# Kernel tuning notes

Measured on AMD Instinct MI355X. Metric: run time of the kernel, lower is better.

Reference implementation:

```python
import jax, jax.numpy as jnp
import numpy as np

N = 100000  # nodes
E = 320000  # edges
G = 64      # graphs in the batch


def setup_inputs() -> dict:
    key = jax.random.key(0)
    ks = jax.random.split(key, 16)
    inp = {
        "x": jax.random.normal(ks[0], (N, 512), dtype=jnp.float32),
        "edge_index": jax.random.randint(ks[1], (2, E), 0, N, dtype=jnp.int64),
        "batch": jnp.sort(jax.random.randint(ks[2], (N,), 0, G, dtype=jnp.int64)),
    }
    # GCNConv weights (in, out) and biases, Glorot-ish scale
    dims = [(512, 256), (256, 128), (128, 64), (64, 32)]
    for i, (din, dout) in enumerate(dims):
        inp[f"w{i+1}"] = jax.random.normal(ks[3 + i], (din, dout), dtype=jnp.float32) / np.sqrt(din)
        inp[f"b{i+1}"] = jnp.zeros((dout,), dtype=jnp.float32)
    inp["lw1"] = jax.random.normal(ks[8], (32, 16), dtype=jnp.float32) / np.sqrt(32.0)
    inp["lb1"] = jnp.zeros((16,), dtype=jnp.float32)
    inp["lw2"] = jax.random.normal(ks[9], (16, 2), dtype=jnp.float32) / np.sqrt(16.0)
    inp["lb2"] = jnpp = jnp.zeros((2,), dtype=jnp.float32)
    return inp


def _gcn_conv(h_in, w, b, src, dst, norm, n):
    # x' = D^-1/2 (A+I) D^-1/2 (X W) + b   (PyG GCNConv default)
    h = h_in @ w                                  # [N, out]
    msg = h[src] * norm[:, None]                  # gather + scale over edges(+self-loops)
    out = jax.ops.segment_sum(msg, dst, num_segments=n)  # scatter-add
    return out + b


def reference(x, edge_index, batch, w1, b1, w2, b2, w3, b3, w4, b4, lw1, lb1, lw2, lb2):
    n = x.shape[0]
    loop = jnp.arange(n, dtype=edge_index.dtype)
    src = jnp.concatenate([edge_index[0], loop])  # add self-loops
    dst = jnp.concatenate([edge_index[1], loop])
    # symmetric normalization: deg counted at dst (col) including self-loops
    deg = jax.ops.segment_sum(jnp.ones_like(dst, dtype=x.dtype), dst, num_segments=n)
    dinv = jnp.where(deg > 0, 1.0 / jnp.sqrt(deg), 0.0)
    norm = dinv[src] * dinv[dst]                  # [E+N]

    h = jax.nn.relu(_gcn_conv(x, w1, b1, src, dst, norm, n))
    h = jax.nn.relu(_gcn_conv(h, w2, b2, src, dst, norm, n))
    h = jax.nn.relu(_gcn_conv(h, w3, b3, src, dst, norm, n))
    h = _gcn_conv(h, w4, b4, src, dst, norm, n)   # [N, 32]

    # global mean pool over graphs
    sums = jax.ops.segment_sum(h, batch, num_segments=G)
    cnt = jax.ops.segment_sum(jnp.ones((n,), dtype=h.dtype), batch, num_segments=G)
    pooled = sums / jnp.maximum(cnt, 1.0)[:, None]  # [G, 32]

    # dropout p=0.8 is identity in eval mode
    out = jax.nn.relu(pooled @ lw1 + lb1) @ lw2 + lb2  # [G, 2]
    return out
```

## Files before the change

### kernel.cpp

```cpp
#include <hip/hip_runtime.h>
#include <cstdint>
#include <cstddef>


typedef __attribute__((ext_vector_type(8))) short s16x8;
typedef __attribute__((ext_vector_type(4))) float f32x4;

__device__ __forceinline__ short2 split2(float f) {
    union { float f; unsigned u; } c; c.f = f;
    short hi = (short)(c.u >> 16);
    union { unsigned u; float f; } h; h.u = c.u & 0xffff0000u;
    union { float f; unsigned u; } r; r.f = f - h.f;
    short lo = (short)(r.u >> 16);
    return make_short2(hi, lo);
}


__global__ void k_count(const int* __restrict__ dst, int E, int* __restrict__ cnt) {
    int e = blockIdx.x * blockDim.x + threadIdx.x;
    if (e < E) atomicAdd(&cnt[dst[e]], 1);
}

__global__ void k_dinv(const int* __restrict__ cnt, int n, float* __restrict__ dinv) {
    int i = blockIdx.x * blockDim.x + threadIdx.x;
    if (i < n) dinv[i] = rsqrtf((float)(cnt[i] + 1));
}


__global__ void k_scan_sums(const int* __restrict__ cnt, int n, int* __restrict__ bsum) {
    __shared__ int s[256];
    int t = threadIdx.x;
    int base = blockIdx.x * 4096 + t * 16;
    int sum = 0;
#pragma unroll
    for (int j = 0; j < 16; ++j) { int i = base + j; if (i < n) sum += cnt[i]; }
    s[t] = sum;
    __syncthreads();
    for (int off = 128; off > 0; off >>= 1) {
        if (t < off) s[t] += s[t + off];
        __syncthreads();
    }
    if (t == 0) bsum[blockIdx.x] = s[0];
}

__global__ void k_scan_offsets(const int* __restrict__ bsum, int nb,
                               int* __restrict__ boff, int* __restrict__ totalp) {
    int t = threadIdx.x;
    int v = (t < nb) ? bsum[t] : 0;
    int x = v;
    for (int off = 1; off < 64; off <<= 1) {
        int y = __shfl_up(x, off);
        if (t >= off) x += y;
    }
    if (t < nb) boff[t] = x - v;
    if (t == 63) *totalp = x;
}

__global__ void k_scan_final(const int* __restrict__ cnt, int n,
                             const int* __restrict__ boff, int* __restrict__ row_ptr) {
    __shared__ int s[256];
    int t = threadIdx.x;
    int base = blockIdx.x * 4096 + t * 16;
    int v[16]; int sum = 0;
#pragma unroll
    for (int j = 0; j < 16; ++j) { int i = base + j; v[j] = (i < n) ? cnt[i] : 0; sum += v[j]; }
    s[t] = sum;
    __syncthreads();
    for (int off = 1; off < 256; off <<= 1) {
        int y = (t >= off) ? s[t - off] : 0;
        __syncthreads();
        s[t] += y;
        __syncthreads();
    }
    int run = boff[blockIdx.x] + ((t == 0) ? 0 : s[t - 1]);
#pragma unroll
    for (int j = 0; j < 16; ++j) {
        int i = base + j;
        if (i < n) row_ptr[i] = run;
        run += v[j];
    }
}

__global__ void k_fill(const int* __restrict__ src, const int* __restrict__ dst, int E,
                       const int* __restrict__ row_ptr, int* __restrict__ cursor,
                       int* __restrict__ csr_src) {
    int e = blockIdx.x * blockDim.x + threadIdx.x;
    if (e >= E) return;
    int d = dst[e];
    int p = atomicAdd(&cursor[d], 1);
    csr_src[row_ptr[d] + p] = src[e];
}


#define SWZ(row, kbyte) ((((row) * 64)) ^ (kbyte) ^ (((row) & 7) << 4))

template <int FM, int FN, int GM, int GN>
__global__ __launch_bounds__(256)
void k_gemm_mfma(const float* __restrict__ A, const float* __restrict__ B,
                 float* __restrict__ C, int M, int K, int N) {
    constexpr int BM = GM * FM * 16;
    constexpr int BN = GN * FN * 16;
    constexpr int BK = 32;
    constexpr int ASZ = BM * BK * 2;
    constexpr int BSZ = BN * BK * 2;
    __shared__ char lds[2 * ASZ + 2 * BSZ];
    char* sAh = lds;
    char* sAl = lds + ASZ;
    char* sBh = lds + 2 * ASZ;
    char* sBl = lds + 2 * ASZ + BSZ;

    const int tid  = threadIdx.x;
    const int lane = tid & 63;
    const int wid  = tid >> 6;
    const int wm   = wid % GM;
    const int wn   = wid / GM;
    const int brow = blockIdx.y * BM;
    const int bcol = blockIdx.x * BN;
    const int l15  = lane & 15;
    const int kb   = ((lane >> 4) * 8) * 2;

    f32x4 acc[FM][FN];
#pragma unroll
    for (int i = 0; i < FM; ++i)
#pragma unroll
        for (int j = 0; j < FN; ++j) acc[i][j] = (f32x4){0.f, 0.f, 0.f, 0.f};

    for (int k0 = 0; k0 < K; k0 += BK) {
#pragma unroll
        for (int slot = tid; slot < BM * 2; slot += 256) {
            int row = slot >> 1, half = slot & 1;
            int gr = brow + row;
            float4 v0, v1, v2, v3;
            if (gr < M) {
                const float4* ap = (const float4*)(A + (size_t)gr * K + k0 + half * 16);
                v0 = ap[0]; v1 = ap[1]; v2 = ap[2]; v3 = ap[3];
            } else {
                v0 = v1 = v2 = v3 = make_float4(0.f, 0.f, 0.f, 0.f);
            }
            s16x8 h0, h1, l0, l1;
            short2 p;
            p = split2(v0.x); h0[0] = p.x; l0[0] = p.y;
            p = split2(v0.y); h0[1] = p.x; l0[1] = p.y;
            p = split2(v0.z); h0[2] = p.x; l0[2] = p.y;
            p = split2(v0.w); h0[3] = p.x; l0[3] = p.y;
            p = split2(v1.x); h0[4] = p.x; l0[4] = p.y;
            p = split2(v1.y); h0[5] = p.x; l0[5] = p.y;
            p = split2(v1.z); h0[6] = p.x; l0[6] = p.y;
            p = split2(v1.w); h0[7] = p.x; l0[7] = p.y;
            p = split2(v2.x); h1[0] = p.x; l1[0] = p.y;
            p = split2(v2.y); h1[1] = p.x; l1[1] = p.y;
            p = split2(v2.z); h1[2] = p.x; l1[2] = p.y;
            p = split2(v2.w); h1[3] = p.x; l1[3] = p.y;
            p = split2(v3.x); h1[4] = p.x; l1[4] = p.y;
            p = split2(v3.y); h1[5] = p.x; l1[5] = p.y;
            p = split2(v3.z); h1[6] = p.x; l1[6] = p.y;
            p = split2(v3.w); h1[7] = p.x; l1[7] = p.y;
            int base = half * 32;
            *(s16x8*)(sAh + SWZ(row, base))      = h0;
            *(s16x8*)(sAh + SWZ(row, base + 16)) = h1;
            *(s16x8*)(sAl + SWZ(row, base))      = l0;
            *(s16x8*)(sAl + SWZ(row, base + 16)) = l1;
        }
#pragma unroll
        for (int slot = tid; slot < BN * 2; slot += 256) {
            int col = slot >> 1, half = slot & 1;
            const float* bp = B + (size_t)(k0 + half * 16) * N + bcol + col;
            s16x8 h0, h1, l0, l1;
#pragma unroll
            for (int j = 0; j < 8; ++j) {
                short2 p = split2(bp[(size_t)j * N]);
                h0[j] = p.x; l0[j] = p.y;
            }
#pragma unroll
            for (int j = 0; j < 8; ++j) {
                short2 p = split2(bp[(size_t)(8 + j) * N]);
                h1[j] = p.x; l1[j] = p.y;
            }
            int base = half * 32;
            *(s16x8*)(sBh + SWZ(col, base))      = h0;
            *(s16x8*)(sBh + SWZ(col, base + 16)) = h1;
            *(s16x8*)(sBl + SWZ(col, base))      = l0;
            *(s16x8*)(sBl + SWZ(col, base + 16)) = l1;
        }
        __syncthreads();

        s16x8 ah[FM], am[FM], bh[FN], bm[FN];
#pragma unroll
        for (int i = 0; i < FM; ++i) {
            int row = wm * FM * 16 + i * 16 + l15;
            ah[i] = *(const s16x8*)(sAh + SWZ(row, kb));
            am[i] = *(const s16x8*)(sAl + SWZ(row, kb));
        }
#pragma unroll
        for (int j = 0; j < FN; ++j) {
            int col = wn * FN * 16 + j * 16 + l15;
            bh[j] = *(const s16x8*)(sBh + SWZ(col, kb));
            bm[j] = *(const s16x8*)(sBl + SWZ(col, kb));
        }
#pragma unroll
        for (int i = 0; i < FM; ++i)
#pragma unroll
            for (int j = 0; j < FN; ++j) {
                acc[i][j] = __builtin_amdgcn_mfma_f32_16x16x32_bf16(ah[i], bh[j], acc[i][j], 0, 0, 0);
                acc[i][j] = __builtin_amdgcn_mfma_f32_16x16x32_bf16(am[i], bh[j], acc[i][j], 0, 0, 0);
                acc[i][j] = __builtin_amdgcn_mfma_f32_16x16x32_bf16(ah[i], bm[j], acc[i][j], 0, 0, 0);
            }
        __syncthreads();
    }

#pragma unroll
    for (int i = 0; i < FM; ++i) {
#pragma unroll
        for (int r = 0; r < 4; ++r) {
            int row = brow + wm * FM * 16 + i * 16 + (lane >> 4) * 4 + r;
            if (row >= M) continue;
#pragma unroll
            for (int j = 0; j < FN; ++j) {
                int col = bcol + wn * FN * 16 + j * 16 + l15;
                C[(size_t)row * N + col] = acc[i][j][r];
            }
        }
    }
}


__global__ void k_agg(const float4* __restrict__ h, const int* __restrict__ row_ptr,
                      const int* __restrict__ csr_src, const float* __restrict__ dinv,
                      const float* __restrict__ bias, float4* __restrict__ out,
                      int n, int f_shift, int do_relu) {
    int idx = blockIdx.x * blockDim.x + threadIdx.x;
    int dout4 = 1 << f_shift;
    int total = n << f_shift;
    if (idx >= total) return;
    int i = idx >> f_shift;
    int f = idx & (dout4 - 1);

    float di = dinv[i];
    float4 hv = h[(size_t)i * dout4 + f];
    float4 acc;
    acc.x = hv.x * di; acc.y = hv.y * di; acc.z = hv.z * di; acc.w = hv.w * di;

    int s0 = row_ptr[i], s1 = row_ptr[i + 1];
    for (int e = s0; e < s1; ++e) {
        int s = csr_src[e];
        float ds = dinv[s];
        float4 v = h[(size_t)s * dout4 + f];
        acc.x += v.x * ds; acc.y += v.y * ds; acc.z += v.z * ds; acc.w += v.w * ds;
    }
    const float4* b4 = (const float4*)bias;
    float4 b = b4[f];
    float4 o;
    o.x = acc.x * di + b.x;
    o.y = acc.y * di + b.y;
    o.z = acc.z * di + b.z;
    o.w = acc.w * di + b.w;
    if (do_relu) {
        o.x = fmaxf(o.x, 0.f); o.y = fmaxf(o.y, 0.f);
        o.z = fmaxf(o.z, 0.f); o.w = fmaxf(o.w, 0.f);
    }
    out[(size_t)i * dout4 + f] = o;
}


__global__ void k_pool(const float* __restrict__ h, const int* __restrict__ batch,
                       int n, float* __restrict__ pooled) {
    int g = blockIdx.x;
    int start, end;
    {
        int lo = 0, hi = n;
        while (lo < hi) { int mid = (lo + hi) >> 1; if (batch[mid] < g) lo = mid + 1; else hi = mid; }
        start = lo;
        lo = start; hi = n;
        while (lo < hi) { int mid = (lo + hi) >> 1; if (batch[mid] < g + 1) lo = mid + 1; else hi = mid; }
        end = lo;
    }
    int f = threadIdx.x & 31;
    int sub = threadIdx.x >> 5;
    float s = 0.f;
    for (int i = start + sub; i < end; i += 8) s += h[(size_t)i * 32 + f];
    __shared__ float red[8][32];
    red[sub][f] = s;
    __syncthreads();
    if (sub == 0) {
        float t = 0.f;
#pragma unroll
        for (int k = 0; k < 8; ++k) t += red[k][f];
        int c = end - start;
        pooled[g * 32 + f] = t / (float)(c > 0 ? c : 1);
    }
}


__global__ void k_mlp(const float* __restrict__ pooled, const float* __restrict__ lw1,
                      const float* __restrict__ lb1, const float* __restrict__ lw2,
                      const float* __restrict__ lb2, float* __restrict__ out, int g_count) {
    int g = threadIdx.x;
    if (g >= g_count) return;
    float p[32];
#pragma unroll
    for (int k = 0; k < 32; ++k) p[k] = pooled[g * 32 + k];
    float hmid[16];
#pragma unroll
    for (int j = 0; j < 16; ++j) {
        float s = lb1[j];
#pragma unroll
        for (int k = 0; k < 32; ++k) s += p[k] * lw1[k * 16 + j];
        hmid[j] = fmaxf(s, 0.f);
    }
#pragma unroll
    for (int o = 0; o < 2; ++o) {
        float s = lb2[o];
#pragma unroll
        for (int k = 0; k < 16; ++k) s += hmid[k] * lw2[k * 2 + o];
        out[g * 2 + o] = s;
    }
}


extern "C" void kernel_launch(void* const* d_in, const int* in_sizes, int n_in,
                              void* d_out, int out_size, void* d_ws, size_t ws_size,
                              hipStream_t stream) {
    const float* x     = (const float*)d_in[0];
    const int*   ei    = (const int*)d_in[1];
    const int*   batch = (const int*)d_in[2];
    const float* w1 = (const float*)d_in[3];  const float* b1 = (const float*)d_in[4];
    const float* w2 = (const float*)d_in[5];  const float* b2 = (const float*)d_in[6];
    const float* w3 = (const float*)d_in[7];  const float* b3 = (const float*)d_in[8];
    const float* w4 = (const float*)d_in[9];  const float* b4 = (const float*)d_in[10];
    const float* lw1 = (const float*)d_in[11]; const float* lb1 = (const float*)d_in[12];
    const float* lw2 = (const float*)d_in[13]; const float* lb2 = (const float*)d_in[14];
    float* out = (float*)d_out;

    const int n = in_sizes[0] / 512;
    const int E = in_sizes[1] / 2;
    const int G = 64;

    const int* src = ei;
    const int* dst = ei + E;

    char* ws = (char*)d_ws;
    size_t off = 0;
    auto alloc = [&](size_t bytes) -> void* {
        void* p = ws + off;
        off = (off + bytes + 255) & ~((size_t)255);
        return p;
    };
    float* bufA    = (float*)alloc((size_t)n * 256 * sizeof(float));
    float* bufB    = (float*)alloc((size_t)n * 256 * sizeof(float));
    int*   cnt     = (int*)alloc((size_t)n * sizeof(int));
    int*   row_ptr = (int*)alloc((size_t)(n + 1) * sizeof(int));
    int*   cursor  = (int*)alloc((size_t)n * sizeof(int));
    int*   csr     = (int*)alloc((size_t)E * sizeof(int));
    float* dinv    = (float*)alloc((size_t)n * sizeof(float));
    float* pooled  = (float*)alloc((size_t)G * 32 * sizeof(float));
    int*   bsum    = (int*)alloc(64 * sizeof(int));
    int*   boff    = (int*)alloc(64 * sizeof(int));
    (void)ws_size;

    hipMemsetAsync(cnt, 0, (size_t)n * sizeof(int), stream);
    hipMemsetAsync(cursor, 0, (size_t)n * sizeof(int), stream);

    const int nscan = (n + 4095) / 4096;

    k_count<<<(E + 255) / 256, 256, 0, stream>>>(dst, E, cnt);
    k_dinv <<<(n + 255) / 256, 256, 0, stream>>>(cnt, n, dinv);
    k_scan_sums   <<<nscan, 256, 0, stream>>>(cnt, n, bsum);
    k_scan_offsets<<<1, 64, 0, stream>>>(bsum, nscan, boff, row_ptr + n);
    k_scan_final  <<<nscan, 256, 0, stream>>>(cnt, n, boff, row_ptr);
    k_fill<<<(E + 255) / 256, 256, 0, stream>>>(src, dst, E, row_ptr, cursor, csr);

    const int gy = (n + 127) / 128;

    k_gemm_mfma<4, 4, 2, 2><<<dim3(2, gy), 256, 0, stream>>>(x, w1, bufA, n, 512, 256);
    k_agg<<<((size_t)n * 64 + 255) / 256, 256, 0, stream>>>(
        (const float4*)bufA, row_ptr, csr, dinv, b1, (float4*)bufB, n, 6, 1);

    k_gemm_mfma<4, 4, 2, 2><<<dim3(1, gy), 256, 0, stream>>>(bufB, w2, bufA, n, 256, 128);
    k_agg<<<((size_t)n * 32 + 255) / 256, 256, 0, stream>>>(
        (const float4*)bufA, row_ptr, csr, dinv, b2, (float4*)bufB, n, 5, 1);

    k_gemm_mfma<4, 2, 2, 2><<<dim3(1, gy), 256, 0, stream>>>(bufB, w3, bufA, n, 128, 64);
    k_agg<<<((size_t)n * 16 + 255) / 256, 256, 0, stream>>>(
        (const float4*)bufA, row_ptr, csr, dinv, b3, (float4*)bufB, n, 4, 1);

    k_gemm_mfma<2, 2, 4, 1><<<dim3(1, gy), 256, 0, stream>>>(bufB, w4, bufA, n, 64, 32);
    k_agg<<<((size_t)n * 8 + 255) / 256, 256, 0, stream>>>(
        (const float4*)bufA, row_ptr, csr, dinv, b4, (float4*)bufB, n, 3, 0);

    k_pool<<<G, 256, 0, stream>>>(bufB, batch, n, pooled);
    k_mlp<<<1, 64, 0, stream>>>(pooled, lw1, lb1, lw2, lb2, out, G);
}
```

Before: 509.5 us.

## Pre-split weights and activations into bf16 hi/lo planes, prefetch GEMM tiles

Weights are split once into transposed bf16 hi/lo planes, so the GEMM no longer does strided per-element B loads with an in-loop split. The aggregation kernels for layers 1-3 now write bf16 hi/lo activations directly, which the next GEMM loads as vectors without converting. The GEMM is restructured with 512-thread blocks, register prefetch of the next K tile overlapping the MFMA work, and full-width N tiles so layer 1 runs one block column instead of two. This adds extra weight-split launches and changes the workspace layout, with bufB aliased into the pAl region.

```diff
diff --git a/kernel.cpp b/kernel.cpp
--- a/kernel.cpp
+++ b/kernel.cpp
@@ -25,7 +25,6 @@
     int i = blockIdx.x * blockDim.x + threadIdx.x;
     if (i < n) dinv[i] = rsqrtf((float)(cnt[i] + 1));
 }
-
 
 __global__ void k_scan_sums(const int* __restrict__ cnt, int n, int* __restrict__ bsum) {
     __shared__ int s[256];
@@ -92,22 +91,36 @@
 }
 
 
+__global__ void k_split_w(const float* __restrict__ w, int N, int total, int kshift,
+                          unsigned short* __restrict__ th, unsigned short* __restrict__ tl) {
+    int idx = blockIdx.x * blockDim.x + threadIdx.x;
+    if (idx >= total) return;
+    int nn = idx >> kshift;
+    int k  = idx & ((1 << kshift) - 1);
+    short2 p = split2(w[(size_t)k * N + nn]);
+    th[idx] = (unsigned short)p.x;
+    tl[idx] = (unsigned short)p.y;
+}
+
+
 #define SWZ(row, kbyte) ((((row) * 64)) ^ (kbyte) ^ (((row) & 7) << 4))
 
-template <int FM, int FN, int GM, int GN>
-__global__ __launch_bounds__(256)
-void k_gemm_mfma(const float* __restrict__ A, const float* __restrict__ B,
-                 float* __restrict__ C, int M, int K, int N) {
-    constexpr int BM = GM * FM * 16;
-    constexpr int BN = GN * FN * 16;
+template <int THREADS, int BM, int BN, int GM, int GN, int FM, int FN, bool SPLIT_A>
+__global__ __launch_bounds__(THREADS)
+void k_gemm(const float* __restrict__ A32,
+            const unsigned short* __restrict__ Ah, const unsigned short* __restrict__ Al,
+            const unsigned short* __restrict__ Bth, const unsigned short* __restrict__ Btl,
+            float* __restrict__ C, int M, int K, int N) {
+    static_assert(GM * GN == THREADS / 64, "waves");
+    static_assert(GM * FM * 16 == BM && GN * FN * 16 == BN, "tile");
     constexpr int BK = 32;
-    constexpr int ASZ = BM * BK * 2;
-    constexpr int BSZ = BN * BK * 2;
-    __shared__ char lds[2 * ASZ + 2 * BSZ];
+    constexpr int APL = BM * BK * 2;
+    constexpr int BPL = BN * BK * 2;
+    __shared__ char lds[2 * APL + 2 * BPL];
     char* sAh = lds;
-    char* sAl = lds + ASZ;
-    char* sBh = lds + 2 * ASZ;
-    char* sBl = lds + 2 * ASZ + BSZ;
+    char* sAl = lds + APL;
+    char* sBh = lds + 2 * APL;
+    char* sBl = lds + 2 * APL + BPL;
 
     const int tid  = threadIdx.x;
     const int lane = tid & 63;
@@ -117,7 +130,76 @@
     const int brow = blockIdx.y * BM;
     const int bcol = blockIdx.x * BN;
     const int l15  = lane & 15;
-    const int kb   = ((lane >> 4) * 8) * 2;
+    const int kb   = (lane >> 4) * 16;
+
+    constexpr int CHA = BM * 4;
+    static_assert(CHA == THREADS, "A chunk = 1/thread");
+    constexpr int CHB = BN * 4;
+    constexpr int NB  = (CHB + THREADS - 1) / THREADS;
+
+    const int arow = tid >> 2;
+    const int akq  = tid & 3;
+    const bool aval = (brow + arow) < M;
+
+    const float*          a32p = A32 + (size_t)(brow + arow) * K + akq * 8;
+    const unsigned short* ahp  = Ah  + (size_t)(brow + arow) * K + akq * 8;
+    const unsigned short* alp  = Al  + (size_t)(brow + arow) * K + akq * 8;
+
+    float4 pa0, pa1, pah, pal;
+    float4 pbh[NB], pbl[NB];
+
+    auto loadA = [&](int k0) {
+        if constexpr (SPLIT_A) {
+            if (aval) {
+                pa0 = *(const float4*)(a32p + k0);
+                pa1 = *(const float4*)(a32p + k0 + 4);
+            } else {
+                pa0 = make_float4(0.f, 0.f, 0.f, 0.f);
+                pa1 = pa0;
+            }
+        } else {
+            if (aval) {
+                pah = *(const float4*)(ahp + k0);
+                pal = *(const float4*)(alp + k0);
+            } else {
+                pah = make_float4(0.f, 0.f, 0.f, 0.f);
+                pal = pah;
+            }
+        }
+    };
+    auto loadB = [&](int k0) {
+#pragma unroll
+        for (int u = 0; u < NB; ++u) {
+            int c = tid + u * THREADS;
+            if (c < CHB) {
+                int col = c >> 2, kq = c & 3;
+                pbh[u] = *(const float4*)(Bth + (size_t)(bcol + col) * K + k0 + kq * 8);
+                pbl[u] = *(const float4*)(Btl + (size_t)(bcol + col) * K + k0 + kq * 8);
+            }
+        }
+    };
+    auto stage = [&]() {
+        if constexpr (SPLIT_A) {
+            float v[8] = {pa0.x, pa0.y, pa0.z, pa0.w, pa1.x, pa1.y, pa1.z, pa1.w};
+            s16x8 h, l;
+#pragma unroll
+            for (int j = 0; j < 8; ++j) { short2 p = split2(v[j]); h[j] = p.x; l[j] = p.y; }
+            *(s16x8*)(sAh + SWZ(arow, akq * 16)) = h;
+            *(s16x8*)(sAl + SWZ(arow, akq * 16)) = l;
+        } else {
+            *(float4*)(sAh + SWZ(arow, akq * 16)) = pah;
+            *(float4*)(sAl + SWZ(arow, akq * 16)) = pal;
+        }
+#pragma unroll
+        for (int u = 0; u < NB; ++u) {
+            int c = tid + u * THREADS;
+            if (c < CHB) {
+                int col = c >> 2, kq = c & 3;
+                *(float4*)(sBh + SWZ(col, kq * 16)) = pbh[u];
+                *(float4*)(sBl + SWZ(col, kq * 16)) = pbl[u];
+            }
+        }
+    };
 
     f32x4 acc[FM][FN];
 #pragma unroll
@@ -125,86 +207,35 @@
 #pragma unroll
         for (int j = 0; j < FN; ++j) acc[i][j] = (f32x4){0.f, 0.f, 0.f, 0.f};
 
-    for (int k0 = 0; k0 < K; k0 += BK) {
-#pragma unroll
-        for (int slot = tid; slot < BM * 2; slot += 256) {
-            int row = slot >> 1, half = slot & 1;
-            int gr = brow + row;
-            float4 v0, v1, v2, v3;
-            if (gr < M) {
-                const float4* ap = (const float4*)(A + (size_t)gr * K + k0 + half * 16);
-                v0 = ap[0]; v1 = ap[1]; v2 = ap[2]; v3 = ap[3];
-            } else {
-                v0 = v1 = v2 = v3 = make_float4(0.f, 0.f, 0.f, 0.f);
-            }
-            s16x8 h0, h1, l0, l1;
-            short2 p;
-            p = split2(v0.x); h0[0] = p.x; l0[0] = p.y;
-            p = split2(v0.y); h0[1] = p.x; l0[1] = p.y;
-            p = split2(v0.z); h0[2] = p.x; l0[2] = p.y;
-            p = split2(v0.w); h0[3] = p.x; l0[3] = p.y;
-            p = split2(v1.x); h0[4] = p.x; l0[4] = p.y;
-            p = split2(v1.y); h0[5] = p.x; l0[5] = p.y;
-            p = split2(v1.z); h0[6] = p.x; l0[6] = p.y;
-            p = split2(v1.w); h0[7] = p.x; l0[7] = p.y;
-            p = split2(v2.x); h1[0] = p.x; l1[0] = p.y;
-            p = split2(v2.y); h1[1] = p.x; l1[1] = p.y;
-            p = split2(v2.z); h1[2] = p.x; l1[2] = p.y;
-            p = split2(v2.w); h1[3] = p.x; l1[3] = p.y;
-            p = split2(v3.x); h1[4] = p.x; l1[4] = p.y;
-            p = split2(v3.y); h1[5] = p.x; l1[5] = p.y;
-            p = split2(v3.z); h1[6] = p.x; l1[6] = p.y;
-            p = split2(v3.w); h1[7] = p.x; l1[7] = p.y;
-            int base = half * 32;
-            *(s16x8*)(sAh + SWZ(row, base))      = h0;
-            *(s16x8*)(sAh + SWZ(row, base + 16)) = h1;
-            *(s16x8*)(sAl + SWZ(row, base))      = l0;
-            *(s16x8*)(sAl + SWZ(row, base + 16)) = l1;
-        }
-#pragma unroll
-        for (int slot = tid; slot < BN * 2; slot += 256) {
-            int col = slot >> 1, half = slot & 1;
-            const float* bp = B + (size_t)(k0 + half * 16) * N + bcol + col;
-            s16x8 h0, h1, l0, l1;
-#pragma unroll
-            for (int j = 0; j < 8; ++j) {
-                short2 p = split2(bp[(size_t)j * N]);
-                h0[j] = p.x; l0[j] = p.y;
-            }
-#pragma unroll
-            for (int j = 0; j < 8; ++j) {
-                short2 p = split2(bp[(size_t)(8 + j) * N]);
-                h1[j] = p.x; l1[j] = p.y;
-            }
-            int base = half * 32;
-            *(s16x8*)(sBh + SWZ(col, base))      = h0;
-            *(s16x8*)(sBh + SWZ(col, base + 16)) = h1;
-            *(s16x8*)(sBl + SWZ(col, base))      = l0;
-            *(s16x8*)(sBl + SWZ(col, base + 16)) = l1;
-        }
+    const int KT = K / BK;
+    loadA(0);
+    loadB(0);
+    for (int t = 0; t < KT; ++t) {
+        stage();
         __syncthreads();
-
-        s16x8 ah[FM], am[FM], bh[FN], bm[FN];
+        if (t + 1 < KT) {
+            loadA((t + 1) * BK);
+            loadB((t + 1) * BK);
+        }
+        s16x8 fah[FM], fam[FM];
 #pragma unroll
         for (int i = 0; i < FM; ++i) {
             int row = wm * FM * 16 + i * 16 + l15;
-            ah[i] = *(const s16x8*)(sAh + SWZ(row, kb));
-            am[i] = *(const s16x8*)(sAl + SWZ(row, kb));
+            fah[i] = *(const s16x8*)(sAh + SWZ(row, kb));
+            fam[i] = *(const s16x8*)(sAl + SWZ(row, kb));
         }
 #pragma unroll
         for (int j = 0; j < FN; ++j) {
             int col = wn * FN * 16 + j * 16 + l15;
-            bh[j] = *(const s16x8*)(sBh + SWZ(col, kb));
-            bm[j] = *(const s16x8*)(sBl + SWZ(col, kb));
-        }
-#pragma unroll
-        for (int i = 0; i < FM; ++i)
-#pragma unroll
-            for (int j = 0; j < FN; ++j) {
-                acc[i][j] = __builtin_amdgcn_mfma_f32_16x16x32_bf16(ah[i], bh[j], acc[i][j], 0, 0, 0);
-                acc[i][j] = __builtin_amdgcn_mfma_f32_16x16x32_bf16(am[i], bh[j], acc[i][j], 0, 0, 0);
-                acc[i][j] = __builtin_amdgcn_mfma_f32_16x16x32_bf16(ah[i], bm[j], acc[i][j], 0, 0, 0);
-            }
+            s16x8 fbh = *(const s16x8*)(sBh + SWZ(col, kb));
+            s16x8 fbm = *(const s16x8*)(sBl + SWZ(col, kb));
+#pragma unroll
+            for (int i = 0; i < FM; ++i) {
+                acc[i][j] = __builtin_amdgcn_mfma_f32_16x16x32_bf16(fah[i], fbh, acc[i][j], 0, 0, 0);
+                acc[i][j] = __builtin_amdgcn_mfma_f32_16x16x32_bf16(fam[i], fbh, acc[i][j], 0, 0, 0);
+                acc[i][j] = __builtin_amdgcn_mfma_f32_16x16x32_bf16(fah[i], fbm, acc[i][j], 0, 0, 0);
+            }
+        }
         __syncthreads();
     }
 
@@ -224,10 +255,51 @@
 }
 
 
+__global__ void k_agg_split(const float4* __restrict__ h, const int* __restrict__ row_ptr,
+                            const int* __restrict__ csr_src, const float* __restrict__ dinv,
+                            const float* __restrict__ bias,
+                            unsigned short* __restrict__ oh, unsigned short* __restrict__ ol,
+                            int n, int f_shift) {
+    int idx = blockIdx.x * blockDim.x + threadIdx.x;
+    int dout4 = 1 << f_shift;
+    int total = n << f_shift;
+    if (idx >= total) return;
+    int i = idx >> f_shift;
+    int f = idx & (dout4 - 1);
+
+    float di = dinv[i];
+    float4 hv = h[(size_t)i * dout4 + f];
+    float4 acc;
+    acc.x = hv.x * di; acc.y = hv.y * di; acc.z = hv.z * di; acc.w = hv.w * di;
+
+    int s0 = row_ptr[i], s1 = row_ptr[i + 1];
+    for (int e = s0; e < s1; ++e) {
+        int s = csr_src[e];
+        float ds = dinv[s];
+        float4 v = h[(size_t)s * dout4 + f];
+        acc.x += v.x * ds; acc.y += v.y * ds; acc.z += v.z * ds; acc.w += v.w * ds;
+    }
+    const float4* b4 = (const float4*)bias;
+    float4 b = b4[f];
+    float4 o;
+    o.x = fmaxf(acc.x * di + b.x, 0.f);
+    o.y = fmaxf(acc.y * di + b.y, 0.f);
+    o.z = fmaxf(acc.z * di + b.z, 0.f);
+    o.w = fmaxf(acc.w * di + b.w, 0.f);
+
+    short2 p0 = split2(o.x), p1 = split2(o.y), p2 = split2(o.z), p3 = split2(o.w);
+    size_t base = ((size_t)i << f_shift << 2) + f * 4;
+    *(ushort4*)(oh + base) = make_ushort4((unsigned short)p0.x, (unsigned short)p1.x,
+                                          (unsigned short)p2.x, (unsigned short)p3.x);
+    *(ushort4*)(ol + base) = make_ushort4((unsigned short)p0.y, (unsigned short)p1.y,
+                                          (unsigned short)p2.y, (unsigned short)p3.y);
+}
+
+
 __global__ void k_agg(const float4* __restrict__ h, const int* __restrict__ row_ptr,
                       const int* __restrict__ csr_src, const float* __restrict__ dinv,
                       const float* __restrict__ bias, float4* __restrict__ out,
-                      int n, int f_shift, int do_relu) {
+                      int n, int f_shift) {
     int idx = blockIdx.x * blockDim.x + threadIdx.x;
     int dout4 = 1 << f_shift;
     int total = n << f_shift;
@@ -254,10 +326,6 @@
     o.y = acc.y * di + b.y;
     o.z = acc.z * di + b.z;
     o.w = acc.w * di + b.w;
-    if (do_relu) {
-        o.x = fmaxf(o.x, 0.f); o.y = fmaxf(o.y, 0.f);
-        o.z = fmaxf(o.z, 0.f); o.w = fmaxf(o.w, 0.f);
-    }
     out[(size_t)i * dout4 + f] = o;
 }
 
@@ -345,8 +413,9 @@
         off = (off + bytes + 255) & ~((size_t)255);
         return p;
     };
-    float* bufA    = (float*)alloc((size_t)n * 256 * sizeof(float));
-    float* bufB    = (float*)alloc((size_t)n * 256 * sizeof(float));
+    float*          bufA = (float*)alloc((size_t)n * 256 * sizeof(float));
+    unsigned short* pAh  = (unsigned short*)alloc((size_t)n * 256 * 2);
+    unsigned short* pAl  = (unsigned short*)alloc((size_t)n * 256 * 2);
     int*   cnt     = (int*)alloc((size_t)n * sizeof(int));
     int*   row_ptr = (int*)alloc((size_t)(n + 1) * sizeof(int));
     int*   cursor  = (int*)alloc((size_t)n * sizeof(int));
@@ -355,13 +424,26 @@
     float* pooled  = (float*)alloc((size_t)G * 32 * sizeof(float));
     int*   bsum    = (int*)alloc(64 * sizeof(int));
     int*   boff    = (int*)alloc(64 * sizeof(int));
+    unsigned short* w1h = (unsigned short*)alloc(256 * 512 * 2);
+    unsigned short* w1l = (unsigned short*)alloc(256 * 512 * 2);
+    unsigned short* w2h = (unsigned short*)alloc(128 * 256 * 2);
+    unsigned short* w2l = (unsigned short*)alloc(128 * 256 * 2);
+    unsigned short* w3h = (unsigned short*)alloc(64 * 128 * 2);
+    unsigned short* w3l = (unsigned short*)alloc(64 * 128 * 2);
+    unsigned short* w4h = (unsigned short*)alloc(32 * 64 * 2);
+    unsigned short* w4l = (unsigned short*)alloc(32 * 64 * 2);
+    float* bufB = (float*)(pAl + (size_t)n * 64);
     (void)ws_size;
 
     hipMemsetAsync(cnt, 0, (size_t)n * sizeof(int), stream);
     hipMemsetAsync(cursor, 0, (size_t)n * sizeof(int), stream);
 
+    k_split_w<<<(256 * 512 + 255) / 256, 256, 0, stream>>>(w1, 256, 256 * 512, 9, w1h, w1l);
+    k_split_w<<<(128 * 256 + 255) / 256, 256, 0, stream>>>(w2, 128, 128 * 256, 8, w2h, w2l);
+    k_split_w<<<(64 * 128 + 255) / 256, 256, 0, stream>>>(w3, 64, 64 * 128, 7, w3h, w3l);
+    k_split_w<<<(32 * 64 + 255) / 256, 256, 0, stream>>>(w4, 32, 32 * 64, 6, w4h, w4l);
+
     const int nscan = (n + 4095) / 4096;
-
     k_count<<<(E + 255) / 256, 256, 0, stream>>>(dst, E, cnt);
     k_dinv <<<(n + 255) / 256, 256, 0, stream>>>(cnt, n, dinv);
     k_scan_sums   <<<nscan, 256, 0, stream>>>(cnt, n, bsum);
@@ -371,21 +453,25 @@
 
     const int gy = (n + 127) / 128;
 
-    k_gemm_mfma<4, 4, 2, 2><<<dim3(2, gy), 256, 0, stream>>>(x, w1, bufA, n, 512, 256);
-    k_agg<<<((size_t)n * 64 + 255) / 256, 256, 0, stream>>>(
-        (const float4*)bufA, row_ptr, csr, dinv, b1, (float4*)bufB, n, 6, 1);
-
-    k_gemm_mfma<4, 4, 2, 2><<<dim3(1, gy), 256, 0, stream>>>(bufB, w2, bufA, n, 256, 128);
-    k_agg<<<((size_t)n * 32 + 255) / 256, 256, 0, stream>>>(
-        (const float4*)bufA, row_ptr, csr, dinv, b2, (float4*)bufB, n, 5, 1);
-
-    k_gemm_mfma<4, 2, 2, 2><<<dim3(1, gy), 256, 0, stream>>>(bufB, w3, bufA, n, 128, 64);
-    k_agg<<<((size_t)n * 16 + 255) / 256, 256, 0, stream>>>(
-        (const float4*)bufA, row_ptr, csr, dinv, b3, (float4*)bufB, n, 4, 1);
-
-    k_gemm_mfma<2, 2, 4, 1><<<dim3(1, gy), 256, 0, stream>>>(bufB, w4, bufA, n, 64, 32);
+    k_gemm<512, 128, 256, 2, 4, 4, 4, true><<<dim3(1, gy), 512, 0, stream>>>(
+        x, pAh, pAl, w1h, w1l, bufA, n, 512, 256);
+    k_agg_split<<<((size_t)n * 64 + 255) / 256, 256, 0, stream>>>(
+        (const float4*)bufA, row_ptr, csr, dinv, b1, pAh, pAl, n, 6);
+
+    k_gemm<512, 128, 128, 2, 4, 4, 2, false><<<dim3(1, gy), 512, 0, stream>>>(
+        nullptr, pAh, pAl, w2h, w2l, bufA, n, 256, 128);
+    k_agg_split<<<((size_t)n * 32 + 255) / 256, 256, 0, stream>>>(
+        (const float4*)bufA, row_ptr, csr, dinv, b2, pAh, pAl, n, 5);
+
+    k_gemm<512, 128, 64, 2, 4, 4, 1, false><<<dim3(1, gy), 512, 0, stream>>>(
+        nullptr, pAh, pAl, w3h, w3l, bufA, n, 128, 64);
+    k_agg_split<<<((size_t)n * 16 + 255) / 256, 256, 0, stream>>>(
+        (const float4*)bufA, row_ptr, csr, dinv, b3, pAh, pAl, n, 4);
+
+    k_gemm<512, 128, 32, 4, 2, 2, 1, false><<<dim3(1, gy), 512, 0, stream>>>(
+        nullptr, pAh, pAl, w4h, w4l, bufA, n, 64, 32);
     k_agg<<<((size_t)n * 8 + 255) / 256, 256, 0, stream>>>(
-        (const float4*)bufA, row_ptr, csr, dinv, b4, (float4*)bufB, n, 3, 0);
+        (const float4*)bufA, row_ptr, csr, dinv, b4, (float4*)bufB, n, 3);
 
     k_pool<<<G, 256, 0, stream>>>(bufB, batch, n, pooled);
     k_mlp<<<1, 64, 0, stream>>>(pooled, lw1, lb1, lw2, lb2, out, G);
```

Result: slower. 638.4 us (+25.3%).
